# Kernel tuning notes

Measured on AMD Instinct MI355X. Metric: run time of the kernel, lower is better.

Reference implementation:

```python
import jax, jax.numpy as jnp
import numpy as np

NEG_INF = -jnp.inf


def _mlp(x, W1, b1, W2, b2, W3, b3):
    h = jax.nn.relu(x @ W1 + b1)
    h = jax.nn.relu(h @ W2 + b2)
    return h @ W3 + b3


def setup_inputs() -> dict:
    key = jax.random.key(0)
    ks = jax.random.split(key, 8)
    B, D, H, A = 65536, 1024, 128, 47
    obs_tensor = jax.random.normal(ks[0], (B, D), jnp.float32)
    action_mask = jax.random.randint(ks[1], (B, 2, A), 0, 2).astype(jnp.int32)
    action_mask = action_mask.at[:, :, 0].set(1)  # pass action always legal
    def lin(k, fan_in, shape):
        s = 1.0 / np.sqrt(fan_in)
        return jax.random.uniform(k, shape, jnp.float32, -s, s)
    W1 = lin(ks[2], D, (D, H)); b1 = lin(ks[3], D, (H,))
    W2 = lin(ks[4], H, (H, H)); b2 = lin(ks[5], H, (H,))
    W3 = lin(ks[6], H, (H, 2 * A)); b3 = lin(ks[7], H, (2 * A,))
    return {"obs_tensor": obs_tensor, "action_mask": action_mask,
            "W1": W1, "b1": b1, "W2": W2, "b2": b2, "W3": W3, "b3": b3}


def reference(obs_tensor, action_mask, W1, b1, W2, b2, W3, b3):
    B = obs_tensor.shape[0]
    A = W3.shape[1] // 2
    logits = _mlp(obs_tensor.reshape(B, -1), W1, b1, W2, b2, W3, b3).reshape(B, 2, A)
    logits = jnp.where(action_mask == 0, NEG_INF, logits)

    fp1 = (action_mask[:, 0].sum(axis=1) == 1) & (action_mask[:, 0, 0] == 1)
    fp2 = (action_mask[:, 1].sum(axis=1) == 1) & (action_mask[:, 1, 0] == 1)

    idx = jnp.arange(A)
    k1, k2 = jax.random.split(jax.random.key(42))
    g1 = jax.random.gumbel(k1, (B, A), jnp.float32)
    g2 = jax.random.gumbel(k2, (B, A), jnp.float32)

    # side 1: when force_pass_2 (and not force_pass_1), index 0 is removed before sampling
    l1 = logits[:, 0]
    l1 = jnp.where((fp2 & ~fp1)[:, None] & (idx[None, :] == 0), NEG_INF, l1)
    a1_sampled = jnp.argmax(l1 + g1, axis=1)
    a1 = jnp.where(fp1, 0, a1_sampled)

    # side 2 extra masking driven by sampled action1 (default branch only)
    switch1 = (a1 >= 1) & (a1 <= 6)
    move1 = (a1 >= 27) & (a1 <= 46)
    extra = (switch1[:, None] & (idx[None, :] == a1[:, None])) | \
            (move1[:, None] & (idx[None, :] >= 27) & (idx[None, :] < 46))
    mask2 = ((fp1 & ~fp2)[:, None] & (idx[None, :] == 0)) | \
            ((~fp1 & ~fp2)[:, None] & extra)
    l2 = jnp.where(mask2, NEG_INF, logits[:, 1])
    a2_sampled = jnp.argmax(l2 + g2, axis=1)
    a2 = jnp.where(fp2, 0, a2_sampled)

    return jnp.stack([a1, a2], axis=1).astype(jnp.int64)
```

## Files before the change

kernel.cpp:

```cpp
#include <hip/hip_runtime.h>

typedef unsigned int u32;
typedef unsigned long long u64;
typedef _Float16 f16;
typedef f16 half8 __attribute__((ext_vector_type(8)));
typedef float f32x4 __attribute__((ext_vector_type(4)));

struct U2 { u32 x, y; };

__host__ __device__ constexpr u32 rotl32(u32 v, int r) {
  return (v << r) | (v >> (32 - r));
}

__host__ __device__ constexpr U2 threefry2x32(u32 k0, u32 k1, u32 c0, u32 c1) {
  u32 ks2 = k0 ^ k1 ^ 0x1BD11BDAu;
  u32 x0 = c0 + k0, x1 = c1 + k1;
#define TFR(r) { x0 += x1; x1 = rotl32(x1, r); x1 ^= x0; }
  TFR(13) TFR(15) TFR(26) TFR(6)
  x0 += k1; x1 += ks2 + 1u;
  TFR(17) TFR(29) TFR(16) TFR(24)
  x0 += ks2; x1 += k0 + 2u;
  TFR(13) TFR(15) TFR(26) TFR(6)
  x0 += k0; x1 += k1 + 3u;
  TFR(17) TFR(29) TFR(16) TFR(24)
  x0 += k1; x1 += ks2 + 4u;
  TFR(13) TFR(15) TFR(26) TFR(6)
  x0 += ks2; x1 += k0 + 5u;
#undef TFR
  return {x0, x1};
}

constexpr U2 SK1 = threefry2x32(0u, 42u, 0u, 0u);
constexpr U2 SK2 = threefry2x32(0u, 42u, 0u, 1u);
constexpr u32 K1A = SK1.x, K1B = SK1.y;
constexpr u32 K2A = SK2.x, K2B = SK2.y;

#define NACT 47

__device__ __forceinline__ float gumbel_at(u32 kA, u32 kB, u32 i) {
  U2 r = threefry2x32(kA, kB, 0u, i);
  u32 bits = r.x ^ r.y;
  float f = __uint_as_float(0x3f800000u | (bits >> 9)) - 1.0f;
  f = fmaxf(f, 1.17549435e-38f);
  return -logf(-logf(f));
}

__device__ __forceinline__ u32 fmono(float f) {
  u32 b = __float_as_uint(f);
  return b ^ ((b & 0x80000000u) ? 0xFFFFFFFFu : 0x80000000u);
}

#define W1H_OFF 0u
#define W1L_OFF 262144u
#define W2H_OFF 524288u
#define W2L_OFF 557056u
#define W3H_OFF 589824u
#define W3L_OFF 614400u
#define WS_NEEDED 638976u

__global__ __launch_bounds__(256)
void prep_weights(const float* __restrict__ W1, const float* __restrict__ W2,
                  const float* __restrict__ W3, char* __restrict__ ws) {
  const int bid = blockIdx.x, t = threadIdx.x;
  if (bid < 512) {
    int idx = bid * 256 + t;
    int col = idx & 127, k = idx >> 7;
    float w = W1[(size_t)k * 128 + col] * 32.0f;
    f16 h = (f16)w;
    f16 l = (f16)((w - (float)h) * 2048.0f);
    u32 addr = (u32)(k >> 6) * 16384u + (u32)(col >> 4) * 2048u +
               (u32)((k >> 5) & 1) * 1024u + (u32)((k >> 3) & 3) * 256u +
               (u32)(col & 15) * 16u + (u32)(k & 7) * 2u;
    *(f16*)(ws + W1H_OFF + addr) = h;
    *(f16*)(ws + W1L_OFF + addr) = l;
  } else if (bid < 576) {
    int idx = (bid - 512) * 256 + t;
    int col = idx & 127, k = idx >> 7;
    float w = W2[(size_t)k * 128 + col] * 32.0f;
    f16 h = (f16)w;
    f16 l = (f16)((w - (float)h) * 2048.0f);
    u32 addr = (u32)(k >> 5) * 8192u + (u32)(col >> 4) * 1024u +
               (u32)((k >> 3) & 3) * 256u + (u32)(col & 15) * 16u + (u32)(k & 7) * 2u;
    *(f16*)(ws + W2H_OFF + addr) = h;
    *(f16*)(ws + W2L_OFF + addr) = l;
  } else {
    int idx = (bid - 576) * 256 + t;
    int col = idx % 96, k = idx / 96;
    float w = (col < 94) ? W3[(size_t)k * 94 + col] * 32.0f : 0.0f;
    f16 h = (f16)w;
    f16 l = (f16)((w - (float)h) * 2048.0f);
    u32 addr = (u32)(k >> 5) * 6144u + (u32)(col >> 4) * 1024u +
               (u32)((k >> 3) & 3) * 256u + (u32)(col & 15) * 16u + (u32)(k & 7) * 2u;
    *(f16*)(ws + W3H_OFF + addr) = h;
    *(f16*)(ws + W3L_OFF + addr) = l;
  }
}

__device__ __forceinline__ f32x4 mfma16(half8 a, half8 b, f32x4 c) {
  return __builtin_amdgcn_mfma_f32_16x16x32_f16(a, b, c, 0, 0, 0);
}

__device__ __forceinline__ void split8(float4 v0, float4 v1, half8& hi, half8& lo) {
  float xs[8] = {v0.x, v0.y, v0.z, v0.w, v1.x, v1.y, v1.z, v1.w};
#pragma unroll
  for (int i = 0; i < 8; i++) {
    f16 h = (f16)xs[i];
    hi[i] = h;
    lo[i] = (f16)((xs[i] - (float)h) * 2048.0f);
  }
}

#define LBAR() do {                                            \
    __builtin_amdgcn_sched_barrier(0);                         \
    asm volatile("s_waitcnt lgkmcnt(0)" ::: "memory");         \
    __builtin_amdgcn_s_barrier();                              \
    __builtin_amdgcn_sched_barrier(0);                         \
  } while (0)

__global__ __launch_bounds__(256, 4)
void fused_mfma(const float* __restrict__ X, const int* __restrict__ AM,
                const float* __restrict__ b1, const float* __restrict__ b2,
                const float* __restrict__ b3, const char* __restrict__ ws,
                int* __restrict__ out) {
  __shared__ __align__(16) char smem[33792];
  const int t = threadIdx.x;
  const int lane = t & 63, wid = t >> 6;
  const int lrow = lane & 15, g = lane >> 4;
  const int wr = wid & 1, wc = wid >> 1;
  const int rowBase = blockIdx.x * 64;
  float* Hb = (float*)smem;

  f32x4 mainA[2][4], crossA[2][4];
#pragma unroll
  for (int ti = 0; ti < 2; ti++)
#pragma unroll
    for (int tc = 0; tc < 4; tc++)
#pragma unroll
      for (int r = 0; r < 4; r++) { mainA[ti][tc][r] = 0.0f; crossA[ti][tc][r] = 0.0f; }

  {
    const int rowS = t >> 2, gq = t & 3;
    const float* xsrc = X + (size_t)(rowBase + rowS) * 1024 + gq * 8;
    const u32 wadr = (u32)rowS * 72u + (u32)gq * 16u;
    const u32 radr0 = (u32)(32 * wr + lrow) * 72u + (u32)g * 16u;
    const u32 radr1 = (u32)(32 * wr + 16 + lrow) * 72u + (u32)g * 16u;
    const char* wbase = ws + W1H_OFF + (u32)(4 * wc) * 2048u + (u32)g * 256u + (u32)lrow * 16u;

    float4 sx0, sx1;
    sx0 = *(const float4*)(xsrc);
    sx1 = *(const float4*)(xsrc + 4);
    {
      half8 h, l;
      split8(sx0, sx1, h, l);
      *(half8*)(smem + wadr) = h;
      *(half8*)(smem + wadr + 4608) = l;
    }
    sx0 = *(const float4*)(xsrc + 32);
    sx1 = *(const float4*)(xsrc + 36);
    LBAR();

    for (int ks = 0; ks < 32; ks++) {
      const u32 cur = (u32)(ks & 1) * 9216u;
      if (ks < 31) {
        const u32 nxt = (u32)((ks + 1) & 1) * 9216u;
        half8 h, l;
        split8(sx0, sx1, h, l);
        *(half8*)(smem + nxt + wadr) = h;
        *(half8*)(smem + nxt + wadr + 4608) = l;
        if (ks < 30) {
          sx0 = *(const float4*)(xsrc + (ks + 2) * 32);
          sx1 = *(const float4*)(xsrc + (ks + 2) * 32 + 4);
        }
      }
      half8 ah0 = *(const half8*)(smem + cur + radr0);
      half8 al0 = *(const half8*)(smem + cur + radr0 + 4608);
      half8 ah1 = *(const half8*)(smem + cur + radr1);
      half8 al1 = *(const half8*)(smem + cur + radr1 + 4608);
      const char* wb = wbase + (u32)(ks >> 1) * 16384u + (u32)(ks & 1) * 1024u;
#pragma unroll
      for (int tc = 0; tc < 4; tc++) {
        half8 bh = *(const half8*)(wb + tc * 2048);
        half8 bl = *(const half8*)(wb + 262144 + tc * 2048);
        mainA[0][tc]  = mfma16(ah0, bh, mainA[0][tc]);
        crossA[0][tc] = mfma16(ah0, bl, crossA[0][tc]);
        crossA[0][tc] = mfma16(al0, bh, crossA[0][tc]);
        mainA[1][tc]  = mfma16(ah1, bh, mainA[1][tc]);
        crossA[1][tc] = mfma16(ah1, bl, crossA[1][tc]);
        crossA[1][tc] = mfma16(al1, bh, crossA[1][tc]);
      }
      LBAR();
    }
  }
#pragma unroll
  for (int ti = 0; ti < 2; ti++)
#pragma unroll
    for (int tc = 0; tc < 4; tc++) {
      const int col = 64 * wc + 16 * tc + lrow;
      const float bb = b1[col];
#pragma unroll
      for (int r = 0; r < 4; r++) {
        const int row = 32 * wr + 16 * ti + 4 * g + r;
        Hb[row * 132 + col] =
            fmaxf((mainA[ti][tc][r] + crossA[ti][tc][r] * 4.8828125e-4f) * 0.03125f + bb,
                  0.0f);
        mainA[ti][tc][r] = 0.0f; crossA[ti][tc][r] = 0.0f;
      }
    }
  __syncthreads();

  {
    const char* wbase = ws + W2H_OFF + (u32)(4 * wc) * 1024u + (u32)g * 256u + (u32)lrow * 16u;
    for (int cc = 0; cc < 4; cc++) {
      half8 ah[2], al[2];
#pragma unroll
      for (int ti = 0; ti < 2; ti++) {
        const float* hp = Hb + (32 * wr + 16 * ti + lrow) * 132 + cc * 32 + 8 * g;
        split8(*(const float4*)hp, *(const float4*)(hp + 4), ah[ti], al[ti]);
      }
      const char* wb = wbase + (u32)cc * 8192u;
#pragma unroll
      for (int tc = 0; tc < 4; tc++) {
        half8 bh = *(const half8*)(wb + tc * 1024);
        half8 bl = *(const half8*)(wb + 32768 + tc * 1024);
#pragma unroll
        for (int ti = 0; ti < 2; ti++) {
          mainA[ti][tc]  = mfma16(ah[ti], bh, mainA[ti][tc]);
          crossA[ti][tc] = mfma16(ah[ti], bl, crossA[ti][tc]);
          crossA[ti][tc] = mfma16(al[ti], bh, crossA[ti][tc]);
        }
      }
    }
  }
  __syncthreads();
#pragma unroll
  for (int ti = 0; ti < 2; ti++)
#pragma unroll
    for (int tc = 0; tc < 4; tc++) {
      const int col = 64 * wc + 16 * tc + lrow;
      const float bb = b2[col];
#pragma unroll
      for (int r = 0; r < 4; r++) {
        const int row = 32 * wr + 16 * ti + 4 * g + r;
        Hb[row * 132 + col] =
            fmaxf((mainA[ti][tc][r] + crossA[ti][tc][r] * 4.8828125e-4f) * 0.03125f + bb,
                  0.0f);
        mainA[ti][tc][r] = 0.0f; crossA[ti][tc][r] = 0.0f;
      }
    }
  __syncthreads();

  f32x4 main3[2][3], cross3[2][3];
#pragma unroll
  for (int ti = 0; ti < 2; ti++)
#pragma unroll
    for (int tc = 0; tc < 3; tc++)
#pragma unroll
      for (int r = 0; r < 4; r++) { main3[ti][tc][r] = 0.0f; cross3[ti][tc][r] = 0.0f; }
  {
    const char* wbase = ws + W3H_OFF + (u32)(3 * wc) * 1024u + (u32)g * 256u + (u32)lrow * 16u;
    for (int cc = 0; cc < 4; cc++) {
      half8 ah[2], al[2];
#pragma unroll
      for (int ti = 0; ti < 2; ti++) {
        const float* hp = Hb + (32 * wr + 16 * ti + lrow) * 132 + cc * 32 + 8 * g;
        split8(*(const float4*)hp, *(const float4*)(hp + 4), ah[ti], al[ti]);
      }
      const char* wb = wbase + (u32)cc * 6144u;
#pragma unroll
      for (int tc = 0; tc < 3; tc++) {
        half8 bh = *(const half8*)(wb + tc * 1024);
        half8 bl = *(const half8*)(wb + 24576 + tc * 1024);
#pragma unroll
        for (int ti = 0; ti < 2; ti++) {
          main3[ti][tc]  = mfma16(ah[ti], bh, main3[ti][tc]);
          cross3[ti][tc] = mfma16(ah[ti], bl, cross3[ti][tc]);
          cross3[ti][tc] = mfma16(al[ti], bh, cross3[ti][tc]);
        }
      }
    }
  }
  __syncthreads();

  float* Ls = (float*)smem;
#pragma unroll
  for (int ti = 0; ti < 2; ti++)
#pragma unroll
    for (int tc = 0; tc < 3; tc++) {
      const int col = 48 * wc + 16 * tc + lrow;
      const float bb = (col < 94) ? b3[col] : 0.0f;
#pragma unroll
      for (int r = 0; r < 4; r++) {
        const int row = 32 * wr + 16 * ti + 4 * g + r;
        Ls[row * 97 + col] =
            (main3[ti][tc][r] + cross3[ti][tc][r] * 4.8828125e-4f) * 0.03125f + bb;
      }
    }
  __syncthreads();

  {
    const int row = 16 * wid + lrow;
    const int q = g;
    const int* amg = AM + (size_t)(rowBase + row) * 94;
    const float* ls = Ls + row * 97;
    const float NI = -__builtin_huge_valf();

    int amv1[12], amv2[12];
    int s0 = 0, s1 = 0;
#pragma unroll
    for (int k = 0; k < 12; k++) {
      const int a = q + 4 * k;
      amv1[k] = (a < NACT) ? amg[a] : 0;
      amv2[k] = (a < NACT) ? amg[NACT + a] : 0;
      s0 += amv1[k]; s1 += amv2[k];
    }
    s0 += __shfl_xor(s0, 16); s0 += __shfl_xor(s0, 32);
    s1 += __shfl_xor(s1, 16); s1 += __shfl_xor(s1, 32);
    const int am0 = amg[0], amN = amg[NACT];
    const bool fp1 = (s0 == 1) && (am0 == 1);
    const bool fp2 = (s1 == 1) && (amN == 1);
    const u32 growA = (u32)(rowBase + row) * 47u;

    u64 best = 0;
#pragma unroll
    for (int k = 0; k < 12; k++) {
      const int a = q + 4 * k;
      if (a >= NACT) break;
      float l = (amv1[k] != 0) ? ls[a] : NI;
      if (fp2 && !fp1 && a == 0) l = NI;
      float v = l + gumbel_at(K1A, K1B, growA + (u32)a);
      u64 key = ((u64)fmono(v) << 6) | (u32)(63 - a);
      if (key > best) best = key;
    }
    u64 o = __shfl_xor(best, 16); if (o > best) best = o;
    o = __shfl_xor(best, 32); if (o > best) best = o;
    const int a1 = fp1 ? 0 : (63 - (int)(best & 63u));

    const bool sw1 = (a1 >= 1) && (a1 <= 6);
    const bool mv1 = (a1 >= 27);
    best = 0;
#pragma unroll
    for (int k = 0; k < 12; k++) {
      const int a = q + 4 * k;
      if (a >= NACT) break;
      float l = (amv2[k] != 0) ? ls[NACT + a] : NI;
      bool extra = (sw1 && a == a1) || (mv1 && a >= 27 && a < 46);
      if ((fp1 && !fp2 && a == 0) || (!fp1 && !fp2 && extra)) l = NI;
      float v = l + gumbel_at(K2A, K2B, growA + (u32)a);
      u64 key = ((u64)fmono(v) << 6) | (u32)(63 - a);
      if (key > best) best = key;
    }
    o = __shfl_xor(best, 16); if (o > best) best = o;
    o = __shfl_xor(best, 32); if (o > best) best = o;
    const int a2 = fp2 ? 0 : (63 - (int)(best & 63u));

    if (q == 0) {
      out[(size_t)(rowBase + row) * 2 + 0] = a1;
      out[(size_t)(rowBase + row) * 2 + 1] = a2;
    }
  }
}

__global__ __launch_bounds__(256)
void fused_policy_v1(const float* __restrict__ X,  const int* __restrict__ AM,
                     const float* __restrict__ W1, const float* __restrict__ b1,
                     const float* __restrict__ W2, const float* __restrict__ b2,
                     const float* __restrict__ W3, const float* __restrict__ b3,
                     int* __restrict__ out) {
  __shared__ alignas(16) char smem[59904];
  float (*HT)[68]   = reinterpret_cast<float (*)[68]>(smem);
  float (*Wst)[128] = reinterpret_cast<float (*)[128]>(smem + 34816);
  float (*Ws3)[96]  = reinterpret_cast<float (*)[96]>(smem + 34816);
  float (*Xt)[68]   = reinterpret_cast<float (*)[68]>(smem + 51200);
  float (*Lsr)[97]  = reinterpret_cast<float (*)[97]>(smem);
  int*   Amf        = reinterpret_cast<int*>(smem + 34816);

  const int t = threadIdx.x;
  const int rowBase = blockIdx.x * 64;
  const int tx = t & 31, ty = t >> 5;
  const int c0 = tx * 4, r0 = ty * 8;

  float accf[8][4]; double accd[8][4];
#pragma unroll
  for (int i = 0; i < 8; i++)
#pragma unroll
    for (int j = 0; j < 4; j++) { accf[i][j] = 0.0f; accd[i][j] = 0.0; }

  for (int k0 = 0; k0 < 1024; k0 += 32) {
#pragma unroll
    for (int i = 0; i < 2; i++) {
      int idx = t + i * 256;
      int row = idx >> 3, kb = (idx & 7) * 4;
      float4 v = *reinterpret_cast<const float4*>(X + (size_t)(rowBase + row) * 1024 + k0 + kb);
      Xt[kb + 0][row] = v.x; Xt[kb + 1][row] = v.y;
      Xt[kb + 2][row] = v.z; Xt[kb + 3][row] = v.w;
    }
#pragma unroll
    for (int i = 0; i < 4; i++) {
      int idx = t + i * 256;
      int kr = idx >> 5, c4 = (idx & 31) * 4;
      *reinterpret_cast<float4*>(&Wst[kr][c4]) =
          *reinterpret_cast<const float4*>(W1 + (size_t)(k0 + kr) * 128 + c4);
    }
    __syncthreads();
#pragma unroll
    for (int kk = 0; kk < 32; kk++) {
      float4 a0 = *reinterpret_cast<const float4*>(&Xt[kk][r0]);
      float4 a1 = *reinterpret_cast<const float4*>(&Xt[kk][r0 + 4]);
      float4 b  = *reinterpret_cast<const float4*>(&Wst[kk][c0]);
      float av[8] = {a0.x, a0.y, a0.z, a0.w, a1.x, a1.y, a1.z, a1.w};
      float bv[4] = {b.x, b.y, b.z, b.w};
#pragma unroll
      for (int i = 0; i < 8; i++)
#pragma unroll
        for (int j = 0; j < 4; j++) accf[i][j] = fmaf(av[i], bv[j], accf[i][j]);
    }
    if ((k0 & 63) == 32) {
#pragma unroll
      for (int i = 0; i < 8; i++)
#pragma unroll
        for (int j = 0; j < 4; j++) { accd[i][j] += (double)accf[i][j]; accf[i][j] = 0.0f; }
    }
    __syncthreads();
  }
  {
    const float4 bv = *reinterpret_cast<const float4*>(b1 + c0);
#pragma unroll
    for (int i = 0; i < 8; i++) {
      HT[c0 + 0][r0 + i] = fmaxf((float)accd[i][0] + bv.x, 0.0f);
      HT[c0 + 1][r0 + i] = fmaxf((float)accd[i][1] + bv.y, 0.0f);
      HT[c0 + 2][r0 + i] = fmaxf((float)accd[i][2] + bv.z, 0.0f);
      HT[c0 + 3][r0 + i] = fmaxf((float)accd[i][3] + bv.w, 0.0f);
    }
  }
  __syncthreads();

#pragma unroll
  for (int i = 0; i < 8; i++)
#pragma unroll
    for (int j = 0; j < 4; j++) { accf[i][j] = 0.0f; accd[i][j] = 0.0; }
  for (int k0 = 0; k0 < 128; k0 += 32) {
#pragma unroll
    for (int i = 0; i < 4; i++) {
      int idx = t + i * 256;
      int kr = idx >> 5, c4 = (idx & 31) * 4;
      *reinterpret_cast<float4*>(&Wst[kr][c4]) =
          *reinterpret_cast<const float4*>(W2 + (size_t)(k0 + kr) * 128 + c4);
    }
    __syncthreads();
#pragma unroll
    for (int kk = 0; kk < 32; kk++) {
      float4 a0 = *reinterpret_cast<const float4*>(&HT[k0 + kk][r0]);
      float4 a1 = *reinterpret_cast<const float4*>(&HT[k0 + kk][r0 + 4]);
      float4 b  = *reinterpret_cast<const float4*>(&Wst[kk][c0]);
      float av[8] = {a0.x, a0.y, a0.z, a0.w, a1.x, a1.y, a1.z, a1.w};
      float bv[4] = {b.x, b.y, b.z, b.w};
#pragma unroll
      for (int i = 0; i < 8; i++)
#pragma unroll
        for (int j = 0; j < 4; j++) accf[i][j] = fmaf(av[i], bv[j], accf[i][j]);
    }
    if ((k0 & 63) == 32) {
#pragma unroll
      for (int i = 0; i < 8; i++)
#pragma unroll
        for (int j = 0; j < 4; j++) { accd[i][j] += (double)accf[i][j]; accf[i][j] = 0.0f; }
    }
    __syncthreads();
  }
  {
    const float4 bv = *reinterpret_cast<const float4*>(b2 + c0);
#pragma unroll
    for (int i = 0; i < 8; i++) {
      HT[c0 + 0][r0 + i] = fmaxf((float)accd[i][0] + bv.x, 0.0f);
      HT[c0 + 1][r0 + i] = fmaxf((float)accd[i][1] + bv.y, 0.0f);
      HT[c0 + 2][r0 + i] = fmaxf((float)accd[i][2] + bv.z, 0.0f);
      HT[c0 + 3][r0 + i] = fmaxf((float)accd[i][3] + bv.w, 0.0f);
    }
  }
  __syncthreads();

  const int c3 = tx * 3;
  float acc3f[8][3]; double acc3d[8][3];
#pragma unroll
  for (int i = 0; i < 8; i++)
#pragma unroll
    for (int j = 0; j < 3; j++) { acc3f[i][j] = 0.0f; acc3d[i][j] = 0.0; }
  for (int k0 = 0; k0 < 128; k0 += 32) {
#pragma unroll
    for (int i = 0; i < 12; i++) {
      int idx = t + i * 256;
      int kr = idx / 96, c = idx - kr * 96;
      Ws3[kr][c] = (c < 94) ? W3[(size_t)(k0 + kr) * 94 + c] : 0.0f;
    }
    __syncthreads();
#pragma unroll
    for (int kk = 0; kk < 32; kk++) {
      float4 a0 = *reinterpret_cast<const float4*>(&HT[k0 + kk][r0]);
      float4 a1 = *reinterpret_cast<const float4*>(&HT[k0 + kk][r0 + 4]);
      float b0 = Ws3[kk][c3], b1v = Ws3[kk][c3 + 1], b2v = Ws3[kk][c3 + 2];
      float av[8] = {a0.x, a0.y, a0.z, a0.w, a1.x, a1.y, a1.z, a1.w};
      float bv3[3] = {b0, b1v, b2v};
#pragma unroll
      for (int i = 0; i < 8; i++)
#pragma unroll
        for (int j = 0; j < 3; j++) acc3f[i][j] = fmaf(av[i], bv3[j], acc3f[i][j]);
    }
    if ((k0 & 63) == 32) {
#pragma unroll
      for (int i = 0; i < 8; i++)
#pragma unroll
        for (int j = 0; j < 3; j++) { acc3d[i][j] += (double)acc3f[i][j]; acc3f[i][j] = 0.0f; }
    }
    __syncthreads();
  }
  {
    float b3v[3];
#pragma unroll
    for (int j = 0; j < 3; j++) b3v[j] = (c3 + j < 94) ? b3[c3 + j] : 0.0f;
#pragma unroll
    for (int i = 0; i < 8; i++)
#pragma unroll
      for (int j = 0; j < 3; j++)
        Lsr[r0 + i][c3 + j] = (float)acc3d[i][j] + b3v[j];
  }
#pragma unroll
  for (int i = 0; i < 24; i++) {
    int idx = t + i * 256;
    if (idx < 64 * 94) Amf[idx] = AM[(size_t)rowBase * 94 + idx];
  }
  __syncthreads();

  if (t < 64) {
    const int row = rowBase + t;
    const float NI = -__builtin_huge_valf();
    const int* am = Amf + t * 94;
    int sum0 = 0, sum1 = 0;
    for (int a = 0; a < NACT; a++) { sum0 += am[a]; sum1 += am[NACT + a]; }
    const bool fp1 = (sum0 == 1) && (am[0] == 1);
    const bool fp2 = (sum1 == 1) && (am[NACT] == 1);
    float bestv = NI; int a1s = 0;
    for (int a = 0; a < NACT; a++) {
      float l = (am[a] != 0) ? Lsr[t][a] : NI;
      if (fp2 && !fp1 && a == 0) l = NI;
      float v = l + gumbel_at(K1A, K1B, (u32)row * 47u + (u32)a);
      if (v > bestv) { bestv = v; a1s = a; }
    }
    const int a1 = fp1 ? 0 : a1s;
    const bool sw1 = (a1 >= 1) && (a1 <= 6);
    const bool mv1 = (a1 >= 27) && (a1 <= 46);
    bestv = NI; int a2s = 0;
    for (int a = 0; a < NACT; a++) {
      float l = (am[NACT + a] != 0) ? Lsr[t][NACT + a] : NI;
      bool extra = (sw1 && a == a1) || (mv1 && a >= 27 && a < 46);
      bool m2 = (fp1 && !fp2 && a == 0) || (!fp1 && !fp2 && extra);
      if (m2) l = NI;
      float v = l + gumbel_at(K2A, K2B, (u32)row * 47u + (u32)a);
      if (v > bestv) { bestv = v; a2s = a; }
    }
    const int a2 = fp2 ? 0 : a2s;
    out[(size_t)row * 2 + 0] = a1;
    out[(size_t)row * 2 + 1] = a2;
  }
}

extern "C" void kernel_launch(void* const* d_in, const int* in_sizes, int n_in,
                              void* d_out, int out_size, void* d_ws, size_t ws_size,
                              hipStream_t stream) {
  const float* X  = (const float*)d_in[0];
  const int*   AM = (const int*)d_in[1];
  const float* W1 = (const float*)d_in[2];
  const float* b1 = (const float*)d_in[3];
  const float* W2 = (const float*)d_in[4];
  const float* b2 = (const float*)d_in[5];
  const float* W3 = (const float*)d_in[6];
  const float* b3 = (const float*)d_in[7];
  int* out = (int*)d_out;

  if (ws_size >= (size_t)WS_NEEDED) {
    prep_weights<<<624, 256, 0, stream>>>(W1, W2, W3, (char*)d_ws);
    fused_mfma<<<1024, 256, 0, stream>>>(X, AM, b1, b2, b3, (const char*)d_ws, out);
  } else {
    fused_policy_v1<<<1024, 256, 0, stream>>>(X, AM, W1, b1, W2, b2, W3, b3, out);
  }
}
```

Measured before the change: 121.2 us.

## Deepen layer-1 prefetch: two-step X lookahead and register-prefetched W1 fragments

The layer-1 K loop is manually unrolled by two so both LDS buffers use constant offsets. X global loads are issued two steps ahead instead of one, and W1 hi/lo fragments for the next step are loaded into registers while the current MFMAs run. The goal is to hide global and L2 latency behind the MFMA chain. This costs more live VGPRs, which may reduce occupancy.

```diff
diff --git a/kernel.cpp b/kernel.cpp
--- a/kernel.cpp
+++ b/kernel.cpp
@@ -146,49 +146,94 @@
     const u32 radr1 = (u32)(32 * wr + 16 + lrow) * 72u + (u32)g * 16u;
     const char* wbase = ws + W1H_OFF + (u32)(4 * wc) * 2048u + (u32)g * 256u + (u32)lrow * 16u;
 
-    float4 sx0, sx1;
-    sx0 = *(const float4*)(xsrc);
-    sx1 = *(const float4*)(xsrc + 4);
+    float4 sxA0, sxA1, sxB0, sxB1;
+    half8 WHc[4], WLc[4];
+
     {
+      float4 t0 = *(const float4*)(xsrc);
+      float4 t1 = *(const float4*)(xsrc + 4);
       half8 h, l;
-      split8(sx0, sx1, h, l);
+      split8(t0, t1, h, l);
       *(half8*)(smem + wadr) = h;
       *(half8*)(smem + wadr + 4608) = l;
     }
-    sx0 = *(const float4*)(xsrc + 32);
-    sx1 = *(const float4*)(xsrc + 36);
+    sxA0 = *(const float4*)(xsrc + 32);  sxA1 = *(const float4*)(xsrc + 36);
+    sxB0 = *(const float4*)(xsrc + 64);  sxB1 = *(const float4*)(xsrc + 68);
+#pragma unroll
+    for (int tc = 0; tc < 4; tc++) {
+      WHc[tc] = *(const half8*)(wbase + tc * 2048);
+      WLc[tc] = *(const half8*)(wbase + 262144 + tc * 2048);
+    }
     LBAR();
 
-    for (int ks = 0; ks < 32; ks++) {
-      const u32 cur = (u32)(ks & 1) * 9216u;
-      if (ks < 31) {
-        const u32 nxt = (u32)((ks + 1) & 1) * 9216u;
+#pragma unroll 1
+    for (int c = 0; c < 32; c += 2) {
+      {
         half8 h, l;
-        split8(sx0, sx1, h, l);
-        *(half8*)(smem + nxt + wadr) = h;
-        *(half8*)(smem + nxt + wadr + 4608) = l;
-        if (ks < 30) {
-          sx0 = *(const float4*)(xsrc + (ks + 2) * 32);
-          sx1 = *(const float4*)(xsrc + (ks + 2) * 32 + 4);
-        }
-      }
-      half8 ah0 = *(const half8*)(smem + cur + radr0);
-      half8 al0 = *(const half8*)(smem + cur + radr0 + 4608);
-      half8 ah1 = *(const half8*)(smem + cur + radr1);
-      half8 al1 = *(const half8*)(smem + cur + radr1 + 4608);
-      const char* wb = wbase + (u32)(ks >> 1) * 16384u + (u32)(ks & 1) * 1024u;
-#pragma unroll
-      for (int tc = 0; tc < 4; tc++) {
-        half8 bh = *(const half8*)(wb + tc * 2048);
-        half8 bl = *(const half8*)(wb + 262144 + tc * 2048);
-        mainA[0][tc]  = mfma16(ah0, bh, mainA[0][tc]);
-        crossA[0][tc] = mfma16(ah0, bl, crossA[0][tc]);
-        crossA[0][tc] = mfma16(al0, bh, crossA[0][tc]);
-        mainA[1][tc]  = mfma16(ah1, bh, mainA[1][tc]);
-        crossA[1][tc] = mfma16(ah1, bl, crossA[1][tc]);
-        crossA[1][tc] = mfma16(al1, bh, crossA[1][tc]);
-      }
-      LBAR();
+        split8(sxA0, sxA1, h, l);
+        *(half8*)(smem + 9216 + wadr) = h;
+        *(half8*)(smem + 9216 + wadr + 4608) = l;
+        if (c + 3 < 32) {
+          sxA0 = *(const float4*)(xsrc + (c + 3) * 32);
+          sxA1 = *(const float4*)(xsrc + (c + 3) * 32 + 4);
+        }
+        half8 ah0 = *(const half8*)(smem + radr0);
+        half8 al0 = *(const half8*)(smem + radr0 + 4608);
+        half8 ah1 = *(const half8*)(smem + radr1);
+        half8 al1 = *(const half8*)(smem + radr1 + 4608);
+#pragma unroll
+        for (int tc = 0; tc < 4; tc++) {
+          mainA[0][tc]  = mfma16(ah0, WHc[tc], mainA[0][tc]);
+          crossA[0][tc] = mfma16(ah0, WLc[tc], crossA[0][tc]);
+          crossA[0][tc] = mfma16(al0, WHc[tc], crossA[0][tc]);
+          mainA[1][tc]  = mfma16(ah1, WHc[tc], mainA[1][tc]);
+          crossA[1][tc] = mfma16(ah1, WLc[tc], crossA[1][tc]);
+          crossA[1][tc] = mfma16(al1, WHc[tc], crossA[1][tc]);
+        }
+        {
+          const char* wb = wbase + (u32)((c + 1) >> 1) * 16384u + (u32)((c + 1) & 1) * 1024u;
+#pragma unroll
+          for (int tc = 0; tc < 4; tc++) {
+            WHc[tc] = *(const half8*)(wb + tc * 2048);
+            WLc[tc] = *(const half8*)(wb + 262144 + tc * 2048);
+          }
+        }
+        LBAR();
+      }
+      {
+        if (c + 2 < 32) {
+          half8 h, l;
+          split8(sxB0, sxB1, h, l);
+          *(half8*)(smem + wadr) = h;
+          *(half8*)(smem + wadr + 4608) = l;
+          if (c + 4 < 32) {
+            sxB0 = *(const float4*)(xsrc + (c + 4) * 32);
+            sxB1 = *(const float4*)(xsrc + (c + 4) * 32 + 4);
+          }
+        }
+        half8 ah0 = *(const half8*)(smem + 9216 + radr0);
+        half8 al0 = *(const half8*)(smem + 9216 + radr0 + 4608);
+        half8 ah1 = *(const half8*)(smem + 9216 + radr1);
+        half8 al1 = *(const half8*)(smem + 9216 + radr1 + 4608);
+#pragma unroll
+        for (int tc = 0; tc < 4; tc++) {
+          mainA[0][tc]  = mfma16(ah0, WHc[tc], mainA[0][tc]);
+          crossA[0][tc] = mfma16(ah0, WLc[tc], crossA[0][tc]);
+          crossA[0][tc] = mfma16(al0, WHc[tc], crossA[0][tc]);
+          mainA[1][tc]  = mfma16(ah1, WHc[tc], mainA[1][tc]);
+          crossA[1][tc] = mfma16(ah1, WLc[tc], crossA[1][tc]);
+          crossA[1][tc] = mfma16(al1, WHc[tc], crossA[1][tc]);
+        }
+        if (c + 2 < 32) {
+          const char* wb = wbase + (u32)((c + 2) >> 1) * 16384u + (u32)((c + 2) & 1) * 1024u;
+#pragma unroll
+          for (int tc = 0; tc < 4; tc++) {
+            WHc[tc] = *(const half8*)(wb + tc * 2048);
+            WLc[tc] = *(const half8*)(wb + 262144 + tc * 2048);
+          }
+        }
+        LBAR();
+      }
     }
   }
 #pragma unroll
```

Result: slower. 155.1 us (+28.0%).
